# Kernel tuning notes

Measured on AMD Instinct MI355X. Metric: run time of the kernel, lower is better.

## Reference

```python
import jax, jax.numpy as jnp
import numpy as np

N_NODES = 100000
N_EDGES = 1000000
NHID = 128
N_CLASSES = 5000


def setup_inputs() -> dict:
    key = jax.random.key(0)
    ks = jax.random.split(key, 8)
    feature = jax.random.normal(ks[0], (N_NODES, NHID), dtype=jnp.float32)
    # Linear weights stored as [in, out] so forward is x @ W + b
    W1 = jax.random.normal(ks[1], (2 * NHID, NHID), dtype=jnp.float32) * (1.0 / np.sqrt(2 * NHID))
    b1 = jnp.zeros((NHID,), dtype=jnp.float32)
    alpha = jnp.full((NHID,), 0.25, dtype=jnp.float32)  # PReLU per-channel init
    W2 = jax.random.normal(ks[2], (NHID, 2), dtype=jnp.float32) * (1.0 / np.sqrt(NHID))
    b2 = jnp.zeros((2,), dtype=jnp.float32)
    row = jax.random.randint(ks[3], (N_EDGES,), 0, N_NODES, dtype=jnp.int64)
    col = jax.random.randint(ks[4], (N_EDGES,), 0, N_NODES, dtype=jnp.int64)
    label = jax.random.randint(ks[5], (N_NODES,), 0, N_CLASSES, dtype=jnp.int64)
    return {"feature": feature, "W1": W1, "b1": b1, "alpha": alpha,
            "W2": W2, "b2": b2, "row": row, "col": col, "label": label}


def reference(feature, W1, b1, alpha, W2, b2, row, col, label):
    # per-edge label: 1 if endpoints share a cluster label
    y = (label[row] == label[col]).astype(jnp.int32)  # [E]
    # edge gather + concat: [E, 2*nhid]
    x = jnp.concatenate([feature[row], feature[col]], axis=1)
    h = x @ W1 + b1                                   # [E, nhid]
    h = jnp.where(h >= 0, h, alpha * h)               # PReLU, per-channel alpha
    logits = h @ W2 + b2                              # [E, 2]
    logp = jax.nn.log_softmax(logits, axis=-1)
    # mean cross-entropy over edges
    loss = -jnp.mean(jnp.take_along_axis(logp, y[:, None], axis=1))
    return loss
```

## Files before the change

### kernel.cpp

```cpp
#include <hip/hip_runtime.h>
#include <hip/hip_bf16.h>

typedef __bf16 bf16_t;
typedef bf16_t bf16x8 __attribute__((ext_vector_type(8)));
typedef float floatx4 __attribute__((ext_vector_type(4)));
typedef float floatx2 __attribute__((ext_vector_type(2)));

#define N_NODES 100000
#define N_EDGES 1000000

#define NBK 98
#define NBP 104
#define NSEG 23
#define SEGCAP 512
#define BCAP (NSEG * SEGCAP)
#define SPCAP 32768
#define SCAT_BLKS 326
#define SCAT_WIN 3072

#define OFF_AUXR  12800000
#define OFF_AUXC  13600000
#define OFF_WT    14400000
#define OFF_WABS  14465536
#define OFF_W1G   14466048
#define OFF_CONST 14466560
#define OFF_RS    14466624ULL
#define OFF_SPILL 24264256ULL
#define OFF_CNT   24526400ULL
#define WS_NEED   24533120ULL
#define CNT_INTS  (NBP * 16 + 16)


__global__ __launch_bounds__(256) void k_prep(const float* __restrict__ W1,
                                              const float* __restrict__ b1,
                                              const float* __restrict__ alpha,
                                              const float* __restrict__ W2,
                                              const float* __restrict__ b2,
                                              bf16_t* __restrict__ WT,
                                              float* __restrict__ wabsp,
                                              float* __restrict__ w1g,
                                              float* __restrict__ constg,
                                              float* __restrict__ out,
                                              int* __restrict__ cnt,
                                              int zero_cnt) {
    const int t = threadIdx.x;
    if (blockIdx.x < 128) {
        int i = blockIdx.x * 256 + t;
        int n = i >> 7, k = i & 127;
        float v = (n < 128) ? W1[k * 128 + n] : W1[(k + 128) * 128 + (n - 128)];
        WT[i] = (bf16_t)v;
        return;
    }
    if (zero_cnt) {
        for (int i = t; i < CNT_INTS; i += 256) cnt[i] = 0;
    }
    __shared__ float w1L[128];
    if (t < 128) {
        float wd = W2[2 * t + 1] - W2[2 * t];
        float al = alpha[t];
        float w1v = wd * (1.f + al) * 0.5f;
        w1L[t] = w1v;
        w1g[t] = w1v;
        int col = (t & 64) + (t & 3) * 16 + ((t >> 2) & 15);
        float wdc = W2[2 * col + 1] - W2[2 * col];
        wabsp[t] = wdc * (1.f - alpha[col]) * 0.5f;
    }
    __syncthreads();
    if (t < 64) {
        float c = fmaf(w1L[t], b1[t], w1L[t + 64] * b1[t + 64]);
#pragma unroll
        for (int m = 32; m >= 1; m >>= 1) c += __shfl_xor(c, m, 64);
        if (t == 0) { *constg = c + (b2[1] - b2[0]); out[0] = 0.f; }
    }
}

__device__ inline unsigned fp4_code(float x) {
    float a = fabsf(x);
    unsigned code = (unsigned)(a > 0.25f) + (a > 0.75f) + (a > 1.25f) + (a > 1.75f)
                  + (a > 2.5f) + (a > 3.5f) + (a > 5.0f);
    return code | (x < 0.f ? 8u : 0u);
}

__global__ __launch_bounds__(256) void k_gemm(const float* __restrict__ F,
                                              const bf16_t* __restrict__ WT,
                                              const float* __restrict__ b1,
                                              const float* __restrict__ w1g,
                                              const int* __restrict__ label,
                                              unsigned char* __restrict__ PQ4,
                                              float2* __restrict__ auxR,
                                              float2* __restrict__ auxC,
                                              const int* __restrict__ row,
                                              const int* __restrict__ col,
                                              long long* __restrict__ RS,
                                              long long* __restrict__ spill,
                                              int* __restrict__ cnt,
                                              int do_scatter) {
    __shared__ __align__(16) char smem[34176];
    const int t = threadIdx.x;

    if (blockIdx.x < SCAT_BLKS) {
        if (!do_scatter) return;
        int* hist = (int*)smem;
        int* lofs = ((int*)smem) + NBP;
        int* base = ((int*)smem) + 2 * NBP;
        const int w0 = blockIdx.x * SCAT_WIN;
        for (int i = t; i < NBP; i += 256) { hist[i] = 0; lofs[i] = 0; }
        __syncthreads();
        int r[12], c[12];
#pragma unroll
        for (int k = 0; k < 12; ++k) {
            int e = w0 + k * 256 + t;
            int es = (e < N_EDGES) ? e : (N_EDGES - 1);
            r[k] = row[es]; c[k] = col[es];
            if (e < N_EDGES) atomicAdd(&hist[r[k] >> 10], 1);
        }
        __syncthreads();
        for (int b = t; b < NBP; b += 256) {
            int n = hist[b];
            base[b] = n ? atomicAdd(&cnt[b * 16], n) : 0;
        }
        __syncthreads();
#pragma unroll
        for (int k = 0; k < 12; ++k) {
            int e = w0 + k * 256 + t;
            if (e < N_EDGES) {
                int b = r[k] >> 10;
                int lo = atomicAdd(&lofs[b], 1);
                int gp = base[b] + lo;
                long long pk = (long long)(unsigned)r[k]
                             | ((long long)(unsigned)c[k] << 32);
                if (gp < BCAP) RS[(size_t)b * BCAP + gp] = pk;
                else {
                    int sp = atomicAdd(&cnt[NBP * 16], 1);
                    if (sp < SPCAP) spill[sp] = pk;
                }
            }
        }
        return;
    }

    bf16x8* Bs = (bf16x8*)smem;
    float (*sP1)[16] = (float (*)[16])(smem + 32768);
    float (*sP2)[16] = (float (*)[16])(smem + 33024);
    const int m0 = (blockIdx.x - SCAT_BLKS) * 32;

    const int w = t >> 6, lane = t & 63;
    const int l15 = lane & 15, quad = lane >> 4;
    const int rw = w >> 1, wq = w & 1;

    const int arow = m0 + rw * 16 + l15;
    const float4* Ar = (const float4*)(F + (size_t)arow * 128 + quad * 8);
    float4 fa[4], fb[4];
#pragma unroll
    for (int s = 0; s < 4; ++s) { fa[s] = Ar[s * 8]; fb[s] = Ar[s * 8 + 1]; }

    float w1v[4], bv[4];
#pragma unroll
    for (int nt = 0; nt < 4; ++nt) {
        int cch = wq * 64 + nt * 16 + l15;
        w1v[nt] = w1g[cch];
        bv[nt] = b1[cch];
    }

    const bf16x8* WT8 = (const bf16x8*)WT;
#pragma unroll
    for (int j = 0; j < 8; ++j) {
        int chunk = j * 256 + t;
        int cr = chunk >> 4, cc = chunk & 15;
        Bs[cr * 16 + (cc ^ (cr & 15))] = WT8[chunk];
    }

    bf16x8 Af[4];
#pragma unroll
    for (int s = 0; s < 4; ++s) {
        bf16x8 v;
        v[0] = (bf16_t)fa[s].x; v[1] = (bf16_t)fa[s].y;
        v[2] = (bf16_t)fa[s].z; v[3] = (bf16_t)fa[s].w;
        v[4] = (bf16_t)fb[s].x; v[5] = (bf16_t)fb[s].y;
        v[6] = (bf16_t)fb[s].z; v[7] = (bf16_t)fb[s].w;
        Af[s] = v;
    }
    __syncthreads();

#pragma unroll
    for (int h = 0; h < 2; ++h) {
        floatx4 acc[4] = {};
#pragma unroll
        for (int s = 0; s < 4; ++s) {
            bf16x8 Bf[4];
#pragma unroll
            for (int nt = 0; nt < 4; ++nt) {
                int cr = wq * 64 + nt * 16 + l15;
                Bf[nt] = Bs[cr * 16 + ((s * 4 + quad) ^ (cr & 15))];
            }
#pragma unroll
            for (int nt = 0; nt < 4; ++nt)
                acc[nt] = __builtin_amdgcn_mfma_f32_16x16x32_bf16(Af[s], Bf[nt], acc[nt], 0, 0, 0);
        }

#pragma unroll
        for (int rr = 0; rr < 4; ++rr) {
            float sv = 0.f;
#pragma unroll
            for (int nt = 0; nt < 4; ++nt) sv = fmaf(w1v[nt], acc[nt][rr], sv);
#pragma unroll
            for (int m = 8; m >= 1; m >>= 1) sv += __shfl_xor(sv, m, 64);
            if (l15 == 0) {
                if (h == 0) sP1[w][quad * 4 + rr] = sv;
                else        sP2[w][quad * 4 + rr] = sv;
            }
        }

#pragma unroll
        for (int rr = 0; rr < 4; ++rr) {
            int g = m0 + rw * 16 + quad * 4 + rr;
            float v0 = acc[0][rr], v1 = acc[1][rr], v2 = acc[2][rr], v3 = acc[3][rr];
            if (h == 0) { v0 += bv[0]; v1 += bv[1]; v2 += bv[2]; v3 += bv[3]; }
            unsigned pk = fp4_code(v0) | (fp4_code(v1) << 4)
                        | (fp4_code(v2) << 8) | (fp4_code(v3) << 12);
            *(unsigned short*)(PQ4 + (size_t)g * 128 + h * 64 + wq * 32 + l15 * 2) =
                (unsigned short)pk;
        }

        if (h == 0) {
            __syncthreads();
#pragma unroll
            for (int j = 0; j < 8; ++j) {
                int chunk = j * 256 + t;
                int cr = chunk >> 4, cc = chunk & 15;
                Bs[cr * 16 + (cc ^ (cr & 15))] = WT8[2048 + chunk];
            }
            __syncthreads();
        }
    }

    __syncthreads();
    if (t < 32) {
        int rw2 = t >> 4, ri = t & 15;
        float s1 = sP1[rw2 * 2][ri] + sP1[rw2 * 2 + 1][ri];
        float s2 = sP2[rw2 * 2][ri] + sP2[rw2 * 2 + 1][ri];
        int g = m0 + rw2 * 16 + ri;
        float lb = __int_as_float(label[g]);
        auxR[g] = make_float2(s1, lb);
        auxC[g] = make_float2(s2, lb);
    }
}

__device__ inline void fp4_decode(unsigned d, unsigned& pe, unsigned& po) {
    unsigned ne = d & 0x0F0F0F0Fu;
    unsigned no = (d >> 4) & 0x0F0F0F0Fu;
    pe = __builtin_amdgcn_perm(0x4C484440u, 0x3C383000u, ne & 0x07070707u)
       | ((ne & 0x08080808u) << 4);
    po = __builtin_amdgcn_perm(0x4C484440u, 0x3C383000u, no & 0x07070707u)
       | ((no & 0x08080808u) << 4);
}

template <int B>
__device__ inline float dw_pair(unsigned p, unsigned q, const float (&W)[32]) {
    unsigned pe, po, qe, qo;
    fp4_decode(p, pe, po);
    fp4_decode(q, qe, qo);
    floatx2 he0 = __builtin_amdgcn_cvt_pk_f32_fp8((int)pe, false)
                + __builtin_amdgcn_cvt_pk_f32_fp8((int)qe, false);
    floatx2 he1 = __builtin_amdgcn_cvt_pk_f32_fp8((int)pe, true)
                + __builtin_amdgcn_cvt_pk_f32_fp8((int)qe, true);
    floatx2 ho0 = __builtin_amdgcn_cvt_pk_f32_fp8((int)po, false)
                + __builtin_amdgcn_cvt_pk_f32_fp8((int)qo, false);
    floatx2 ho1 = __builtin_amdgcn_cvt_pk_f32_fp8((int)po, true)
                + __builtin_amdgcn_cvt_pk_f32_fp8((int)qo, true);
    float s;
    s = fabsf(he0[0]) * W[B + 0];
    s = fmaf(fabsf(he0[1]), W[B + 1], s);
    s = fmaf(fabsf(he1[0]), W[B + 2], s);
    s = fmaf(fabsf(he1[1]), W[B + 3], s);
    s = fmaf(fabsf(ho0[0]), W[B + 4], s);
    s = fmaf(fabsf(ho0[1]), W[B + 5], s);
    s = fmaf(fabsf(ho1[0]), W[B + 6], s);
    s = fmaf(fabsf(ho1[1]), W[B + 7], s);
    return s;
}

__device__ inline int2 ldRS(const long long* __restrict__ seg, int off,
                            int lane, int segN) {
    int ei = off + (lane >> 2);
    ei = (ei < segN) ? ei : (segN - 1);
    long long v = __builtin_nontemporal_load(&seg[ei]);
    return make_int2((int)(unsigned)(v & 0xFFFFFFFFll),
                     (int)(unsigned)((unsigned long long)v >> 32));
}

__device__ inline void ldG(const unsigned char* __restrict__ PQ4,
                           const float2* __restrict__ auxR,
                           const float2* __restrict__ auxC, int2 rc, int sub,
                           uint4& P, uint4& Q, float2& A) {
    P = *(const uint4*)(PQ4 + (unsigned)rc.x * 128u + (unsigned)sub * 16u);
    Q = *(const uint4*)(PQ4 + (unsigned)rc.y * 128u + 64u + (unsigned)sub * 16u);
    A = (sub & 1) ? auxC[rc.y] : auxR[rc.x];
}

__device__ inline float edge16(uint4 P, uint4 Q, float2 A, int off, int segN,
                               int lane, int sub, const float (&W)[32],
                               float CB) {
    float s = dw_pair<0>(P.x, Q.x, W) + dw_pair<8>(P.y, Q.y, W)
            + dw_pair<16>(P.z, Q.z, W) + dw_pair<24>(P.w, Q.w, W);
    s += __shfl_xor(s, 1, 64);
    s += __shfl_xor(s, 2, 64);
    int gb = lane & ~3;
    float s2 = __shfl(A.x, gb + 1, 64);
    float lc = __shfl(A.y, gb + 1, 64);
    float D = A.x + s2 + CB + s;
    float sgn = (__float_as_int(A.y) == __float_as_int(lc)) ? -D : D;
    float loss = fmaxf(sgn, 0.f) + __logf(1.f + __expf(-fabsf(sgn)));
    bool valid = (sub == 0) && (off + (lane >> 2) < segN);
    return valid ? loss : 0.f;
}

__global__ __launch_bounds__(256) void k_edge_bkt(const unsigned char* __restrict__ PQ4,
                                                  const float2* __restrict__ auxR,
                                                  const float2* __restrict__ auxC,
                                                  const float* __restrict__ wabsp,
                                                  const float* __restrict__ constg,
                                                  const long long* __restrict__ RS,
                                                  const long long* __restrict__ spill,
                                                  const int* __restrict__ cnt,
                                                  float* __restrict__ out) {
    const int lane = threadIdx.x & 63;
    const int w = threadIdx.x >> 6;
    const int sub = lane & 3;

    const long long* seg; int segN;
    {
        const int blk = blockIdx.x;
        if (blk < NBP * NSEG) {
            int bk = blk % NBP, sg = blk / NBP;
            int cc = cnt[bk * 16]; if (cc > BCAP) cc = BCAP;
            int st = sg * SEGCAP;
            segN = cc - st; if (segN < 0) segN = 0; if (segN > SEGCAP) segN = SEGCAP;
            seg = RS + (size_t)bk * BCAP + st;
        } else {
            int sc = cnt[NBP * 16]; if (sc > SPCAP) sc = SPCAP;
            int si = blk - NBP * NSEG;
            int per = (sc + 7) >> 3;
            int st = si * per;
            segN = sc - st; if (segN < 0) segN = 0; if (segN > per) segN = per;
            seg = spill + st;
        }
    }

    float W[32];
    const float* wb = wabsp + sub * 32;
#pragma unroll
    for (int d = 0; d < 4; ++d) {
        const float* wd = wb + d * 8;
        W[d * 8 + 0] = wd[0]; W[d * 8 + 1] = wd[2];
        W[d * 8 + 2] = wd[4]; W[d * 8 + 3] = wd[6];
        W[d * 8 + 4] = wd[1]; W[d * 8 + 5] = wd[3];
        W[d * 8 + 6] = wd[5]; W[d * 8 + 7] = wd[7];
    }
    const float CB = *constg;

    const int off0 = w * 16;
    const int nMy = (segN > off0) ? ((segN - off0 + 63) >> 6) : 0;
    float accw = 0.f;
    if (nMy > 0) {
        int2 rcCur = ldRS(seg, off0, lane, segN);
        int2 rcNext = (nMy > 1) ? ldRS(seg, off0 + 64, lane, segN) : rcCur;
        uint4 Pc, Qc; float2 Ac;
        ldG(PQ4, auxR, auxC, rcCur, sub, Pc, Qc, Ac);
        for (int k = 0; k < nMy; ++k) {
            int2 rcN2 = (k + 2 < nMy) ? ldRS(seg, off0 + (k + 2) * 64, lane, segN)
                                      : rcCur;
            uint4 Pn, Qn; float2 An;
            int2 rcG = (k + 1 < nMy) ? rcNext : rcCur;
            ldG(PQ4, auxR, auxC, rcG, sub, Pn, Qn, An);
            __builtin_amdgcn_sched_barrier(0);
            accw += edge16(Pc, Qc, Ac, off0 + k * 64, segN, lane, sub, W, CB);
            rcCur = rcNext; rcNext = rcN2;
            Pc = Pn; Qc = Qn; Ac = An;
        }
    }

#pragma unroll
    for (int m = 32; m >= 1; m >>= 1) accw += __shfl_xor(accw, m, 64);
    __shared__ float sdata[4];
    if (lane == 0) sdata[w] = accw;
    __syncthreads();
    if (threadIdx.x == 0) {
        float ssum = (sdata[0] + sdata[1]) + (sdata[2] + sdata[3]);
        atomicAdd(out, ssum * (1.f / (float)N_EDGES));
    }
}

__global__ __launch_bounds__(256) void k_edge_loss(const unsigned char* __restrict__ PQ4,
                                                   const float2* __restrict__ auxR,
                                                   const float2* __restrict__ auxC,
                                                   const float* __restrict__ wabsp,
                                                   const float* __restrict__ constg,
                                                   const int* __restrict__ row,
                                                   const int* __restrict__ col,
                                                   float* __restrict__ out) {
    const int lane = threadIdx.x & 63;
    const int wid = (blockIdx.x * blockDim.x + threadIdx.x) >> 6;
    const int e0 = wid * 64;
    const int sub = lane & 3, eidx = lane >> 2;

    float W[32];
    const float* wb = wabsp + sub * 32;
#pragma unroll
    for (int d = 0; d < 4; ++d) {
        const float* wd = wb + d * 8;
        W[d * 8 + 0] = wd[0]; W[d * 8 + 1] = wd[2];
        W[d * 8 + 2] = wd[4]; W[d * 8 + 3] = wd[6];
        W[d * 8 + 4] = wd[1]; W[d * 8 + 5] = wd[3];
        W[d * 8 + 6] = wd[5]; W[d * 8 + 7] = wd[7];
    }
    const float CB = *constg;

    int el = e0 + lane;
    if (el >= N_EDGES) el = N_EDGES - 1;
    int rowreg = row[el];
    int colreg = col[el];

    int rV[4], cV[4];
#pragma unroll
    for (int c = 0; c < 4; ++c) {
        rV[c] = __shfl(rowreg, c * 16 + eidx, 64);
        cV[c] = __shfl(colreg, c * 16 + eidx, 64);
    }
    int alow = ((lane >> 5) << 4) + (lane & 15);
    int ra1 = __shfl(rowreg, alow, 64), ca1 = __shfl(colreg, alow, 64);
    int ra2 = __shfl(rowreg, 32 + alow, 64), ca2 = __shfl(colreg, 32 + alow, 64);
    float2 A1 = (lane & 16) ? auxC[ca1] : auxR[ra1];
    float2 A2 = (lane & 16) ? auxC[ca2] : auxR[ra2];

    uint4 P[4], Q[4];
#pragma unroll
    for (int c = 0; c < 4; ++c) {
        P[c] = *(const uint4*)(PQ4 + (unsigned)rV[c] * 128u + (unsigned)sub * 16u);
        Q[c] = *(const uint4*)(PQ4 + (unsigned)cV[c] * 128u + 64u + (unsigned)sub * 16u);
    }
    __builtin_amdgcn_sched_barrier(0);

    float acc = 0.f;
#pragma unroll
    for (int c = 0; c < 4; ++c) {
        float s = dw_pair<0>(P[c].x, Q[c].x, W)
                + dw_pair<8>(P[c].y, Q[c].y, W)
                + dw_pair<16>(P[c].z, Q[c].z, W)
                + dw_pair<24>(P[c].w, Q[c].w, W);
        s += __shfl_xor(s, 1, 64);
        s += __shfl_xor(s, 2, 64);
        const float2 Av = (c < 2) ? A1 : A2;
        const int base = (c & 1) * 32;
        float s1 = __shfl(Av.x, base + eidx, 64);
        float s2 = __shfl(Av.x, base + 16 + eidx, 64);
        float lr = __shfl(Av.y, base + eidx, 64);
        float lc = __shfl(Av.y, base + 16 + eidx, 64);
        float D = s1 + s2 + CB + s;
        float sgn = (__float_as_int(lr) == __float_as_int(lc)) ? -D : D;
        float loss = fmaxf(sgn, 0.f) + __logf(1.f + __expf(-fabsf(sgn)));
        int e = e0 + c * 16 + eidx;
        acc += (sub == 0 && e < N_EDGES) ? loss : 0.f;
    }

#pragma unroll
    for (int m = 32; m >= 1; m >>= 1) acc += __shfl_xor(acc, m, 64);
    __shared__ float sdata[4];
    int l64 = threadIdx.x & 63;
    int wv = threadIdx.x >> 6;
    if (l64 == 0) sdata[wv] = acc;
    __syncthreads();
    if (threadIdx.x == 0) {
        float ssum = (sdata[0] + sdata[1]) + (sdata[2] + sdata[3]);
        atomicAdd(out, ssum * (1.f / (float)N_EDGES));
    }
}

extern "C" void kernel_launch(void* const* d_in, const int* in_sizes, int n_in,
                              void* d_out, int out_size, void* d_ws, size_t ws_size,
                              hipStream_t stream) {
    const float* feature = (const float*)d_in[0];
    const float* W1      = (const float*)d_in[1];
    const float* b1      = (const float*)d_in[2];
    const float* alpha   = (const float*)d_in[3];
    const float* W2      = (const float*)d_in[4];
    const float* b2      = (const float*)d_in[5];
    const int*   row     = (const int*)d_in[6];
    const int*   col     = (const int*)d_in[7];
    const int*   label   = (const int*)d_in[8];
    float* out = (float*)d_out;

    char* ws = (char*)d_ws;
    unsigned char* PQ4 = (unsigned char*)(ws);
    float2* auxR = (float2*)(ws + OFF_AUXR);
    float2* auxC = (float2*)(ws + OFF_AUXC);
    bf16_t* WT   = (bf16_t*)(ws + OFF_WT);
    float* wabsp = (float*)(ws + OFF_WABS);
    float* w1g   = (float*)(ws + OFF_W1G);
    float* constg= (float*)(ws + OFF_CONST);

    const int bkt = (ws_size >= WS_NEED) ? 1 : 0;
    long long* RS    = (long long*)(ws + (bkt ? OFF_RS    : 0));
    long long* spill = (long long*)(ws + (bkt ? OFF_SPILL : 0));
    int*       cnt   = (int*)(ws + (bkt ? OFF_CNT    : 0));

    k_prep<<<129, 256, 0, stream>>>(W1, b1, alpha, W2, b2, WT, wabsp, w1g,
                                    constg, out, cnt, bkt);
    k_gemm<<<SCAT_BLKS + 3125, 256, 0, stream>>>(feature, WT, b1, w1g, label,
                                                 PQ4, auxR, auxC, row, col,
                                                 RS, spill, cnt, bkt);
    if (bkt) {
        k_edge_bkt<<<NBP * NSEG + 8, 256, 0, stream>>>(PQ4, auxR, auxC,
                                                       wabsp, constg, RS, spill,
                                                       cnt, out);
    } else {
        k_edge_loss<<<3907, 256, 0, stream>>>(PQ4, auxR, auxC, wabsp,
                                              constg, row, col, out);
    }
}
```

Baseline: 180.6 us.

## Stage per-bucket row-node features in LDS and shrink buckets to 512 nodes

The row-node buckets shrink from 1024 to 512 nodes, and the segment/capacity constants and workspace offsets are changed to match. Each edge block now copies the bucket's 512 row-node feature halves and aux values into shared memory. Row gathers then read from LDS, and only column features are fetched from global memory. This cuts scattered global traffic for the row half, at the cost of a per-block staging copy and a barrier. It also adds a risk: if PQ4 or auxR is not sized for the last bucket, the staging copy can read past N_NODES (bucket 195 covers nodes up to 100351).

After: 170.2 us. 1.06x faster.

```diff
diff --git a/kernel.cpp b/kernel.cpp
--- a/kernel.cpp
+++ b/kernel.cpp
@@ -9,12 +9,14 @@
 #define N_NODES 100000
 #define N_EDGES 1000000
 
-#define NBK 98
-#define NBP 104
-#define NSEG 23
-#define SEGCAP 512
+#define BSHIFT 9
+#define WIN 512
+#define NBK 196
+#define NBP 200
+#define NSEG 6
+#define SEGCAP 1024
 #define BCAP (NSEG * SEGCAP)
-#define SPCAP 32768
+#define SPCAP 16384
 #define SCAT_BLKS 326
 #define SCAT_WIN 3072
 
@@ -25,9 +27,9 @@
 #define OFF_W1G   14466048
 #define OFF_CONST 14466560
 #define OFF_RS    14466624ULL
-#define OFF_SPILL 24264256ULL
-#define OFF_CNT   24526400ULL
-#define WS_NEED   24533120ULL
+#define OFF_SPILL 24297024ULL
+#define OFF_CNT   24428096ULL
+#define WS_NEED   24440960ULL
 #define CNT_INTS  (NBP * 16 + 16)
 
 
@@ -112,7 +114,7 @@
             int e = w0 + k * 256 + t;
             int es = (e < N_EDGES) ? e : (N_EDGES - 1);
             r[k] = row[es]; c[k] = col[es];
-            if (e < N_EDGES) atomicAdd(&hist[r[k] >> 10], 1);
+            if (e < N_EDGES) atomicAdd(&hist[r[k] >> BSHIFT], 1);
         }
         __syncthreads();
         for (int b = t; b < NBP; b += 256) {
@@ -124,7 +126,7 @@
         for (int k = 0; k < 12; ++k) {
             int e = w0 + k * 256 + t;
             if (e < N_EDGES) {
-                int b = r[k] >> 10;
+                int b = r[k] >> BSHIFT;
                 int lo = atomicAdd(&lofs[b], 1);
                 int gp = base[b] + lo;
                 long long pk = (long long)(unsigned)r[k]
@@ -289,6 +291,36 @@
                      (int)(unsigned)((unsigned long long)v >> 32));
 }
 
+__device__ inline void ldGc(const unsigned char* __restrict__ PQ4,
+                            const float2* __restrict__ auxC, int2 rc, int sub,
+                            uint4& Q, float2& A) {
+    Q = *(const uint4*)(PQ4 + (unsigned)rc.y * 128u + 64u + (unsigned)sub * 16u);
+    A = make_float2(0.f, 0.f);
+    if (sub & 1) A = auxC[rc.y];
+}
+
+__device__ inline float edge16s(const uint4* __restrict__ rowT,
+                                const float2* __restrict__ auxT, int b0node,
+                                int2 rc, uint4 Q, float2 Acol, int off,
+                                int segN, int lane, int sub,
+                                const float (&W)[32], float CB) {
+    int rl = rc.x - b0node;
+    uint4 P = rowT[rl * 4 + sub];
+    float2 A = (sub & 1) ? Acol : auxT[rl];
+    float s = dw_pair<0>(P.x, Q.x, W) + dw_pair<8>(P.y, Q.y, W)
+            + dw_pair<16>(P.z, Q.z, W) + dw_pair<24>(P.w, Q.w, W);
+    s += __shfl_xor(s, 1, 64);
+    s += __shfl_xor(s, 2, 64);
+    int gb = lane & ~3;
+    float s2 = __shfl(A.x, gb + 1, 64);
+    float lc = __shfl(A.y, gb + 1, 64);
+    float D = A.x + s2 + CB + s;
+    float sgn = (__float_as_int(A.y) == __float_as_int(lc)) ? -D : D;
+    float loss = fmaxf(sgn, 0.f) + __logf(1.f + __expf(-fabsf(sgn)));
+    bool valid = (sub == 0) && (off + (lane >> 2) < segN);
+    return valid ? loss : 0.f;
+}
+
 __device__ inline void ldG(const unsigned char* __restrict__ PQ4,
                            const float2* __restrict__ auxR,
                            const float2* __restrict__ auxC, int2 rc, int sub,
@@ -316,36 +348,21 @@
 }
 
 __global__ __launch_bounds__(256) void k_edge_bkt(const unsigned char* __restrict__ PQ4,
-                                                  const float2* __restrict__ auxR,
-                                                  const float2* __restrict__ auxC,
+                                                  const float2* __restrict__ auxRg,
+                                                  const float2* __restrict__ auxCg,
                                                   const float* __restrict__ wabsp,
                                                   const float* __restrict__ constg,
                                                   const long long* __restrict__ RS,
                                                   const long long* __restrict__ spill,
                                                   const int* __restrict__ cnt,
                                                   float* __restrict__ out) {
-    const int lane = threadIdx.x & 63;
-    const int w = threadIdx.x >> 6;
+    __shared__ __align__(16) unsigned char rowBytes[WIN * 64];
+    __shared__ float2 auxT[WIN];
+    __shared__ float sdata[4];
+    const int t = threadIdx.x;
+    const int lane = t & 63;
+    const int w = t >> 6;
     const int sub = lane & 3;
-
-    const long long* seg; int segN;
-    {
-        const int blk = blockIdx.x;
-        if (blk < NBP * NSEG) {
-            int bk = blk % NBP, sg = blk / NBP;
-            int cc = cnt[bk * 16]; if (cc > BCAP) cc = BCAP;
-            int st = sg * SEGCAP;
-            segN = cc - st; if (segN < 0) segN = 0; if (segN > SEGCAP) segN = SEGCAP;
-            seg = RS + (size_t)bk * BCAP + st;
-        } else {
-            int sc = cnt[NBP * 16]; if (sc > SPCAP) sc = SPCAP;
-            int si = blk - NBP * NSEG;
-            int per = (sc + 7) >> 3;
-            int st = si * per;
-            segN = sc - st; if (segN < 0) segN = 0; if (segN > per) segN = per;
-            seg = spill + st;
-        }
-    }
 
     float W[32];
     const float* wb = wabsp + sub * 32;
@@ -358,34 +375,79 @@
         W[d * 8 + 6] = wd[5]; W[d * 8 + 7] = wd[7];
     }
     const float CB = *constg;
-
-    const int off0 = w * 16;
-    const int nMy = (segN > off0) ? ((segN - off0 + 63) >> 6) : 0;
     float accw = 0.f;
-    if (nMy > 0) {
-        int2 rcCur = ldRS(seg, off0, lane, segN);
-        int2 rcNext = (nMy > 1) ? ldRS(seg, off0 + 64, lane, segN) : rcCur;
-        uint4 Pc, Qc; float2 Ac;
-        ldG(PQ4, auxR, auxC, rcCur, sub, Pc, Qc, Ac);
-        for (int k = 0; k < nMy; ++k) {
-            int2 rcN2 = (k + 2 < nMy) ? ldRS(seg, off0 + (k + 2) * 64, lane, segN)
-                                      : rcCur;
-            uint4 Pn, Qn; float2 An;
-            int2 rcG = (k + 1 < nMy) ? rcNext : rcCur;
-            ldG(PQ4, auxR, auxC, rcG, sub, Pn, Qn, An);
-            __builtin_amdgcn_sched_barrier(0);
-            accw += edge16(Pc, Qc, Ac, off0 + k * 64, segN, lane, sub, W, CB);
-            rcCur = rcNext; rcNext = rcN2;
-            Pc = Pn; Qc = Qn; Ac = An;
+
+    const int blk = blockIdx.x;
+    if (blk < NBP * NSEG) {
+        const int bk = blk % NBP, sg = blk / NBP;
+        int cc = cnt[bk * 16]; if (cc > BCAP) cc = BCAP;
+        int st = sg * SEGCAP;
+        int segN = cc - st; if (segN < 0) segN = 0; if (segN > SEGCAP) segN = SEGCAP;
+        if (segN > 0) {
+            const long long* seg = RS + (size_t)bk * BCAP + st;
+            const int b0node = bk << BSHIFT;
+
+            uint4* rowT = (uint4*)rowBytes;
+            for (int c = t; c < WIN * 4; c += 256) {
+                int node = c >> 2, part = c & 3;
+                rowT[c] = *(const uint4*)(PQ4 + (size_t)(b0node + node) * 128
+                                          + (unsigned)part * 16u);
+            }
+            for (int i = t; i < WIN; i += 256) auxT[i] = auxRg[b0node + i];
+            __syncthreads();
+
+            const int off0 = w * 16;
+            const int nMy = (segN > off0) ? ((segN - off0 + 63) >> 6) : 0;
+            if (nMy > 0) {
+                int2 rc0 = ldRS(seg, off0, lane, segN);
+                int2 rc1 = (nMy > 1) ? ldRS(seg, off0 + 64, lane, segN) : rc0;
+                uint4 Q0; float2 A0;
+                ldGc(PQ4, auxCg, rc0, sub, Q0, A0);
+                for (int k = 0; k < nMy; ++k) {
+                    int2 rc2 = (k + 2 < nMy) ? ldRS(seg, off0 + (k + 2) * 64, lane, segN)
+                                             : rc0;
+                    uint4 Q1; float2 A1;
+                    int2 rcG = (k + 1 < nMy) ? rc1 : rc0;
+                    ldGc(PQ4, auxCg, rcG, sub, Q1, A1);
+                    __builtin_amdgcn_sched_barrier(0);
+                    accw += edge16s((const uint4*)rowBytes, auxT, b0node, rc0,
+                                    Q0, A0, off0 + k * 64, segN, lane, sub, W, CB);
+                    rc0 = rc1; rc1 = rc2; Q0 = Q1; A0 = A1;
+                }
+            }
+        }
+    } else {
+        int sc = cnt[NBP * 16]; if (sc > SPCAP) sc = SPCAP;
+        int si = blk - NBP * NSEG;
+        int per = (sc + 7) >> 3;
+        int st = si * per;
+        int segN = sc - st; if (segN < 0) segN = 0; if (segN > per) segN = per;
+        const long long* seg = spill + st;
+        const int off0 = w * 16;
+        const int nMy = (segN > off0) ? ((segN - off0 + 63) >> 6) : 0;
+        if (nMy > 0) {
+            int2 rc0 = ldRS(seg, off0, lane, segN);
+            int2 rc1 = (nMy > 1) ? ldRS(seg, off0 + 64, lane, segN) : rc0;
+            uint4 P0, Q0; float2 A0;
+            ldG(PQ4, auxRg, auxCg, rc0, sub, P0, Q0, A0);
+            for (int k = 0; k < nMy; ++k) {
+                int2 rc2 = (k + 2 < nMy) ? ldRS(seg, off0 + (k + 2) * 64, lane, segN)
+                                         : rc0;
+                uint4 P1, Q1; float2 A1;
+                int2 rcG = (k + 1 < nMy) ? rc1 : rc0;
+                ldG(PQ4, auxRg, auxCg, rcG, sub, P1, Q1, A1);
+                __builtin_amdgcn_sched_barrier(0);
+                accw += edge16(P0, Q0, A0, off0 + k * 64, segN, lane, sub, W, CB);
+                rc0 = rc1; rc1 = rc2; P0 = P1; Q0 = Q1; A0 = A1;
+            }
         }
     }
 
 #pragma unroll
     for (int m = 32; m >= 1; m >>= 1) accw += __shfl_xor(accw, m, 64);
-    __shared__ float sdata[4];
     if (lane == 0) sdata[w] = accw;
     __syncthreads();
-    if (threadIdx.x == 0) {
+    if (t == 0) {
         float ssum = (sdata[0] + sdata[1]) + (sdata[2] + sdata[3]);
         atomicAdd(out, ssum * (1.f / (float)N_EDGES));
     }
```
